# Kernel optimization log

Hardware: AMD Instinct MI355X
Metric: run time of the kernel (lower is better)

The kernel has to match this reference:

```python
import jax, jax.numpy as jnp
import numpy as np

B, T, F = 8192, 30, 16
H1, H2 = 64, 32


def _lstm(x, Wih, Whh, b):
    """PyTorch-convention LSTM (gate order i,f,g,o). x: [B,T,I] -> (ys [B,T,H], hT [B,H])."""
    H = Whh.shape[1]
    h0 = jnp.zeros((x.shape[0], H), x.dtype)

    def step(carry, xt):
        h, c = carry
        z = xt @ Wih.T + h @ Whh.T + b  # [B,4H]
        i, f, g, o = jnp.split(z, 4, axis=-1)
        c = jax.nn.sigmoid(f) * c + jax.nn.sigmoid(i) * jnp.tanh(g)
        h = jax.nn.sigmoid(o) * jnp.tanh(c)
        return (h, c), h

    (hT, _), ys = jax.lax.scan(step, (h0, h0), jnp.swapaxes(x, 0, 1))
    return jnp.swapaxes(ys, 0, 1), hT


def setup_inputs() -> dict:
    key = jax.random.key(0)
    ks = jax.random.split(key, 16)
    s = 0.1  # small init scale for numerical sanity
    return {
        "x": jax.random.normal(ks[0], (B, T, F), jnp.float32),
        "Wih1": jax.random.normal(ks[1], (4 * H1, F), jnp.float32) * s,
        "Whh1": jax.random.normal(ks[2], (4 * H1, H1), jnp.float32) * s,
        "b1": jax.random.normal(ks[3], (4 * H1,), jnp.float32) * s,
        "Wih2": jax.random.normal(ks[4], (4 * H2, H1), jnp.float32) * s,
        "Whh2": jax.random.normal(ks[5], (4 * H2, H2), jnp.float32) * s,
        "b2": jax.random.normal(ks[6], (4 * H2,), jnp.float32) * s,
        "Wih3": jax.random.normal(ks[7], (4 * H2, H2), jnp.float32) * s,
        "Whh3": jax.random.normal(ks[8], (4 * H2, H2), jnp.float32) * s,
        "b3": jax.random.normal(ks[9], (4 * H2,), jnp.float32) * s,
        "Wih4": jax.random.normal(ks[10], (4 * H1, H2), jnp.float32) * s,
        "Whh4": jax.random.normal(ks[11], (4 * H1, H1), jnp.float32) * s,
        "b4": jax.random.normal(ks[12], (4 * H1,), jnp.float32) * s,
        "Wout": jax.random.normal(ks[13], (F, H1), jnp.float32) * s,
        "bout": jax.random.normal(ks[14], (F,), jnp.float32) * s,
    }


def reference(x, Wih1, Whh1, b1, Wih2, Whh2, b2, Wih3, Whh3, b3, Wih4, Whh4, b4, Wout, bout):
    ys1, _ = _lstm(x, Wih1, Whh1, b1)          # encoder LSTM(64)
    _, latent = _lstm(ys1, Wih2, Whh2, b2)      # encoder LSTM(32) -> final hidden [B,32]
    repeated = jnp.broadcast_to(latent[:, None, :], (latent.shape[0], T, latent.shape[1]))
    ys3, _ = _lstm(repeated, Wih3, Whh3, b3)    # decoder LSTM(32)
    ys4, _ = _lstm(ys3, Wih4, Whh4, b4)         # decoder LSTM(64)
    return ys4 @ Wout.T + bout                  # [B,T,F]
```

## Files before the change

### kernel.cpp

```cpp
#include <hip/hip_runtime.h>


#define TT 30
#define FF 16
#define NT 768

typedef unsigned short u16t;
typedef __attribute__((ext_vector_type(8))) short short8;
typedef __attribute__((ext_vector_type(4))) short short4v;
typedef __attribute__((ext_vector_type(4))) float floatx4;

#define MFMA(a, b, c) __builtin_amdgcn_mfma_f32_16x16x32_bf16(a, b, c, 0, 0, 0)

#if __has_builtin(__builtin_amdgcn_exp2f)
#define EXP2(x) __builtin_amdgcn_exp2f(x)
#else
#define EXP2(x) exp2f(x)
#endif

template <int P> struct IC { static constexpr int v = P; };

__device__ __forceinline__ float rcpf(float v) { return __builtin_amdgcn_rcpf(v); }
__device__ __forceinline__ u16t f2bf(float f) {
  unsigned int u = __float_as_uint(f);
  u = (u + 0x7FFFu + ((u >> 16) & 1u)) >> 16;
  return (u16t)u;
}
__device__ __forceinline__ short8 ldFragS(const float* p, float s) {
  const float4 lo = *(const float4*)p;
  const float4 hi = *(const float4*)(p + 4);
  short8 r;
  r[0] = (short)f2bf(lo.x * s); r[1] = (short)f2bf(lo.y * s);
  r[2] = (short)f2bf(lo.z * s); r[3] = (short)f2bf(lo.w * s);
  r[4] = (short)f2bf(hi.x * s); r[5] = (short)f2bf(hi.y * s);
  r[6] = (short)f2bf(hi.z * s); r[7] = (short)f2bf(hi.w * s);
  return r;
}
__device__ __forceinline__ float cellUp(const floatx4 acc, float& c) {
  float ei = EXP2(-acc[0]);
  float ef = EXP2(-acc[1]);
  float eg = EXP2(-acc[2]);
  float eo = EXP2(-acc[3]);
  float fv = rcpf(1.f + ef);
  float P  = (1.f - eg) * rcpf((1.f + ei) * (1.f + eg));
  c = fv * c + P;
  float ec = EXP2(-2.885390082f * c);
  return (1.f - ec) * rcpf((1.f + eo) * (1.f + ec));
}

__global__ __launch_bounds__(NT, 3) void lstm_ae_mfma8(
    const float* __restrict__ x,
    const float* __restrict__ Wih1, const float* __restrict__ Whh1, const float* __restrict__ b1,
    const float* __restrict__ Wih2, const float* __restrict__ Whh2, const float* __restrict__ b2,
    const float* __restrict__ Wih3, const float* __restrict__ Whh3, const float* __restrict__ b3,
    const float* __restrict__ Wih4, const float* __restrict__ Whh4, const float* __restrict__ b4,
    const float* __restrict__ Wout, const float* __restrict__ bout,
    float* __restrict__ out)
{
  __shared__ __align__(16) u16t xAll[32 * 968];
  __shared__ __align__(16) u16t aB[32 * 264];

  const int t = threadIdx.x;
  const int w = t >> 6, lane = t & 63;
  const int q = lane >> 4, n = lane & 15;
  const int q8 = q * 8;
  const int bBase = blockIdx.x * 32;
  const int nlo = n >> 2, ngt = n & 3;
  const int r0 = n * 264, r1 = (n + 16) * 264;
  const int x0 = n * 968, x1 = (n + 16) * 968;
  const bool isZ1 = (w < 8);
  const int u = w & 3;

  const float L1 = 1.442695041f, L2 = 2.885390082f;
  const float sA = (ngt == 2) ? L2 : L1;

  for (int i = t; i < 32 * 264; i += NT) aB[i] = 0;
  {
    const float* xb = x + (size_t)bBase * (TT * FF);
    for (int i4 = t; i4 < 3840; i4 += NT) {
      int e = i4 * 4;
      int b = e / 480, r = e - b * 480;
      int stp = r >> 4, f = r & 15;
      float4 v = *(const float4*)&xb[e];
      short4v s4 = { (short)f2bf(v.x), (short)f2bf(v.y), (short)f2bf(v.z), (short)f2bf(v.w) };
      *(short4v*)&xAll[b * 968 + stp * 32 + f] = s4;
    }
    for (int i = t; i < 15360; i += NT) {
      int b = i / 480, r = i - b * 480;
      int stp = r >> 4, f = r & 15;
      xAll[b * 968 + stp * 32 + 16 + f] = 0;
    }
  }
  const short8 z8 = { 0, 0, 0, 0, 0, 0, 0, 0 };
  short8 wAf[2][3]; floatx4 biasA[2];
  if (isZ1) {
#pragma unroll
    for (int tt = 0; tt < 2; ++tt) {
      int T = w + 8 * tt;
      int row = ngt * 64 + T * 4 + nlo;
      wAf[tt][0] = z8;
      if (q < 2) wAf[tt][0] = ldFragS(&Wih1[row * 16 + q8], sA);
      wAf[tt][1] = ldFragS(&Whh1[row * 64 + q8], sA);
      wAf[tt][2] = ldFragS(&Whh1[row * 64 + 32 + q8], sA);
#pragma unroll
      for (int r = 0; r < 4; ++r) biasA[tt][r] = b1[r * 64 + T * 4 + q] * (r == 2 ? L2 : L1);
    }
  } else {
#pragma unroll
    for (int tt = 0; tt < 2; ++tt) {
      int T = 2 * u + tt;
      int row = ngt * 32 + T * 4 + nlo;
      wAf[tt][0] = ldFragS(&Wih2[row * 64 + q8], sA);
      wAf[tt][1] = ldFragS(&Wih2[row * 64 + 32 + q8], sA);
      wAf[tt][2] = ldFragS(&Whh2[row * 32 + q8], sA);
#pragma unroll
      for (int r = 0; r < 4; ++r) biasA[tt][r] = b2[r * 32 + T * 4 + q] * (r == 2 ? L2 : L1);
    }
  }
  __syncthreads();

  float cA[2][2] = {{0.f, 0.f}, {0.f, 0.f}};
  short8 bxN[2];

  if (isZ1) {
    const short8 bx0 = *(const short8*)&xAll[x0 + q8];
    const short8 bx1 = *(const short8*)&xAll[x1 + q8];
#pragma unroll
    for (int tt = 0; tt < 2; ++tt) {
      floatx4 a0 = biasA[tt], a1 = biasA[tt];
      a0 = MFMA(wAf[tt][0], bx0, a0);
      a1 = MFMA(wAf[tt][0], bx1, a1);
      aB[r0 + (w + 8 * tt) * 4 + q] = f2bf(cellUp(a0, cA[0][tt]));
      aB[r1 + (w + 8 * tt) * 4 + q] = f2bf(cellUp(a1, cA[1][tt]));
    }
    bxN[0] = *(const short8*)&xAll[x0 + 32 + q8];
    bxN[1] = *(const short8*)&xAll[x1 + 32 + q8];
  }
  __syncthreads();

  auto stepA = [&](int st, auto pc) {
    constexpr int p = decltype(pc)::v;
    const short8 h1a0 = *(const short8*)&aB[r0 + p * 64 + q8];
    const short8 h1b0 = *(const short8*)&aB[r0 + p * 64 + 32 + q8];
    const short8 h1a1 = *(const short8*)&aB[r1 + p * 64 + q8];
    const short8 h1b1 = *(const short8*)&aB[r1 + p * 64 + 32 + q8];
    if (isZ1) {
#pragma unroll
      for (int tt = 0; tt < 2; ++tt) {
        floatx4 a0 = biasA[tt], a1 = biasA[tt];
        a0 = MFMA(wAf[tt][0], bxN[0], a0);
        a1 = MFMA(wAf[tt][0], bxN[1], a1);
        a0 = MFMA(wAf[tt][1], h1a0, a0);
        a1 = MFMA(wAf[tt][1], h1a1, a1);
        a0 = MFMA(wAf[tt][2], h1b0, a0);
        a1 = MFMA(wAf[tt][2], h1b1, a1);
        aB[r0 + (1 - p) * 64 + (w + 8 * tt) * 4 + q] = f2bf(cellUp(a0, cA[0][tt]));
        aB[r1 + (1 - p) * 64 + (w + 8 * tt) * 4 + q] = f2bf(cellUp(a1, cA[1][tt]));
      }
      const int nx = (st + 2 < TT) ? st + 2 : TT - 1;
      bxN[0] = *(const short8*)&xAll[x0 + nx * 32 + q8];
      bxN[1] = *(const short8*)&xAll[x1 + nx * 32 + q8];
    } else {
      const short8 h20 = *(const short8*)&aB[r0 + 128 + (1 - p) * 32 + q8];
      const short8 h21 = *(const short8*)&aB[r1 + 128 + (1 - p) * 32 + q8];
#pragma unroll
      for (int tt = 0; tt < 2; ++tt) {
        floatx4 a0 = biasA[tt], a1 = biasA[tt];
        a0 = MFMA(wAf[tt][0], h1a0, a0);
        a1 = MFMA(wAf[tt][0], h1a1, a1);
        a0 = MFMA(wAf[tt][1], h1b0, a0);
        a1 = MFMA(wAf[tt][1], h1b1, a1);
        a0 = MFMA(wAf[tt][2], h20, a0);
        a1 = MFMA(wAf[tt][2], h21, a1);
        aB[r0 + 128 + p * 32 + (2 * u + tt) * 4 + q] = f2bf(cellUp(a0, cA[0][tt]));
        aB[r1 + 128 + p * 32 + (2 * u + tt) * 4 + q] = f2bf(cellUp(a1, cA[1][tt]));
      }
    }
    __syncthreads();
  };
  for (int st = 0; st < 28; st += 2) { stepA(st, IC<0>{}); stepA(st + 1, IC<1>{}); }
  stepA(28, IC<0>{});
  if (!isZ1) {
    const short8 h1a0 = *(const short8*)&aB[r0 + 64 + q8];
    const short8 h1b0 = *(const short8*)&aB[r0 + 96 + q8];
    const short8 h1a1 = *(const short8*)&aB[r1 + 64 + q8];
    const short8 h1b1 = *(const short8*)&aB[r1 + 96 + q8];
    const short8 h20  = *(const short8*)&aB[r0 + 128 + q8];
    const short8 h21  = *(const short8*)&aB[r1 + 128 + q8];
#pragma unroll
    for (int tt = 0; tt < 2; ++tt) {
      floatx4 a0 = biasA[tt], a1 = biasA[tt];
      a0 = MFMA(wAf[tt][0], h1a0, a0);
      a1 = MFMA(wAf[tt][0], h1a1, a1);
      a0 = MFMA(wAf[tt][1], h1b0, a0);
      a1 = MFMA(wAf[tt][1], h1b1, a1);
      a0 = MFMA(wAf[tt][2], h20, a0);
      a1 = MFMA(wAf[tt][2], h21, a1);
      aB[r0 + 160 + (2 * u + tt) * 4 + q] = f2bf(cellUp(a0, cA[0][tt]));
      aB[r1 + 160 + (2 * u + tt) * 4 + q] = f2bf(cellUp(a1, cA[1][tt]));
    }
  }
  __syncthreads();

  short8 wBf[2][3]; floatx4 biasB[2];
  short8 wof[2]; floatx4 biasO;
  short8 blat[2];
  if (isZ1) {
#pragma unroll
    for (int tt = 0; tt < 2; ++tt) {
      int T = w + 8 * tt;
      int row = ngt * 64 + T * 4 + nlo;
      wBf[tt][0] = ldFragS(&Wih4[row * 32 + q8], sA);
      wBf[tt][1] = ldFragS(&Whh4[row * 64 + q8], sA);
      wBf[tt][2] = ldFragS(&Whh4[row * 64 + 32 + q8], sA);
#pragma unroll
      for (int r = 0; r < 4; ++r) biasB[tt][r] = b4[r * 64 + T * 4 + q] * (r == 2 ? L2 : L1);
    }
    wof[0] = ldFragS(&Wout[n * 64 + q8], 1.f);
    wof[1] = ldFragS(&Wout[n * 64 + 32 + q8], 1.f);
    biasO = *(const floatx4*)&bout[q * 4];
  } else {
#pragma unroll
    for (int tt = 0; tt < 2; ++tt) {
      int T = 2 * u + tt;
      int row = ngt * 32 + T * 4 + nlo;
      wBf[tt][0] = ldFragS(&Wih3[row * 32 + q8], sA);
      wBf[tt][1] = ldFragS(&Whh3[row * 32 + q8], sA);
#pragma unroll
      for (int r = 0; r < 4; ++r) biasB[tt][r] = b3[r * 32 + T * 4 + q] * (r == 2 ? L2 : L1);
    }
    blat[0] = *(const short8*)&aB[r0 + 160 + q8];
    blat[1] = *(const short8*)&aB[r1 + 160 + q8];
  }
  for (int i = t; i < 2048; i += NT) aB[(i >> 6) * 264 + 64 + (i & 63)] = 0;
  __syncthreads();

  float cB[2][2] = {{0.f, 0.f}, {0.f, 0.f}};

  if (!isZ1) {
#pragma unroll
    for (int tt = 0; tt < 2; ++tt) {
      floatx4 a0 = biasB[tt], a1 = biasB[tt];
      a0 = MFMA(wBf[tt][0], blat[0], a0);
      a1 = MFMA(wBf[tt][0], blat[1], a1);
      aB[r0 + 192 + (2 * u + tt) * 4 + q] = f2bf(cellUp(a0, cB[0][tt]));
      aB[r1 + 192 + (2 * u + tt) * 4 + q] = f2bf(cellUp(a1, cB[1][tt]));
    }
  }
  __syncthreads();

  auto stepB = [&](int st, auto pc) {
    constexpr int p = decltype(pc)::v;
    const short8 h30 = *(const short8*)&aB[r0 + 192 + p * 32 + q8];
    const short8 h31 = *(const short8*)&aB[r1 + 192 + p * 32 + q8];
    if (isZ1) {
      const short8 h4a0 = *(const short8*)&aB[r0 + (1 - p) * 64 + q8];
      const short8 h4b0 = *(const short8*)&aB[r0 + (1 - p) * 64 + 32 + q8];
      const short8 h4a1 = *(const short8*)&aB[r1 + (1 - p) * 64 + q8];
      const short8 h4b1 = *(const short8*)&aB[r1 + (1 - p) * 64 + 32 + q8];
#pragma unroll
      for (int tt = 0; tt < 2; ++tt) {
        floatx4 a0 = biasB[tt], a1 = biasB[tt];
        a0 = MFMA(wBf[tt][0], h30, a0);
        a1 = MFMA(wBf[tt][0], h31, a1);
        a0 = MFMA(wBf[tt][1], h4a0, a0);
        a1 = MFMA(wBf[tt][1], h4a1, a1);
        a0 = MFMA(wBf[tt][2], h4b0, a0);
        a1 = MFMA(wBf[tt][2], h4b1, a1);
        aB[r0 + p * 64 + (w + 8 * tt) * 4 + q] = f2bf(cellUp(a0, cB[0][tt]));
        aB[r1 + p * 64 + (w + 8 * tt) * 4 + q] = f2bf(cellUp(a1, cB[1][tt]));
      }
      if (st > 0 && w == ((st - 1) & 7)) {
        floatx4 y0 = biasO, y1 = biasO;
        y0 = MFMA(wof[0], h4a0, y0);
        y1 = MFMA(wof[0], h4a1, y1);
        y0 = MFMA(wof[1], h4b0, y0);
        y1 = MFMA(wof[1], h4b1, y1);
        *(floatx4*)&out[((size_t)(bBase + n) * TT + (st - 1)) * FF + q * 4] = y0;
        *(floatx4*)&out[((size_t)(bBase + n + 16) * TT + (st - 1)) * FF + q * 4] = y1;
      }
    } else {
#pragma unroll
      for (int tt = 0; tt < 2; ++tt) {
        floatx4 a0 = biasB[tt], a1 = biasB[tt];
        a0 = MFMA(wBf[tt][0], blat[0], a0);
        a1 = MFMA(wBf[tt][0], blat[1], a1);
        a0 = MFMA(wBf[tt][1], h30, a0);
        a1 = MFMA(wBf[tt][1], h31, a1);
        aB[r0 + 192 + (1 - p) * 32 + (2 * u + tt) * 4 + q] = f2bf(cellUp(a0, cB[0][tt]));
        aB[r1 + 192 + (1 - p) * 32 + (2 * u + tt) * 4 + q] = f2bf(cellUp(a1, cB[1][tt]));
      }
    }
    __syncthreads();
  };
  for (int st = 0; st < 28; st += 2) { stepB(st, IC<0>{}); stepB(st + 1, IC<1>{}); }
  stepB(28, IC<0>{});
  if (isZ1) {
    const short8 h30  = *(const short8*)&aB[r0 + 224 + q8];
    const short8 h31  = *(const short8*)&aB[r1 + 224 + q8];
    const short8 h4a0 = *(const short8*)&aB[r0 + q8];
    const short8 h4b0 = *(const short8*)&aB[r0 + 32 + q8];
    const short8 h4a1 = *(const short8*)&aB[r1 + q8];
    const short8 h4b1 = *(const short8*)&aB[r1 + 32 + q8];
#pragma unroll
    for (int tt = 0; tt < 2; ++tt) {
      floatx4 a0 = biasB[tt], a1 = biasB[tt];
      a0 = MFMA(wBf[tt][0], h30, a0);
      a1 = MFMA(wBf[tt][0], h31, a1);
      a0 = MFMA(wBf[tt][1], h4a0, a0);
      a1 = MFMA(wBf[tt][1], h4a1, a1);
      a0 = MFMA(wBf[tt][2], h4b0, a0);
      a1 = MFMA(wBf[tt][2], h4b1, a1);
      aB[r0 + 64 + (w + 8 * tt) * 4 + q] = f2bf(cellUp(a0, cB[0][tt]));
      aB[r1 + 64 + (w + 8 * tt) * 4 + q] = f2bf(cellUp(a1, cB[1][tt]));
    }
    if (w == 4) {
      floatx4 y0 = biasO, y1 = biasO;
      y0 = MFMA(wof[0], h4a0, y0);
      y1 = MFMA(wof[0], h4a1, y1);
      y0 = MFMA(wof[1], h4b0, y0);
      y1 = MFMA(wof[1], h4b1, y1);
      *(floatx4*)&out[((size_t)(bBase + n) * TT + 28) * FF + q * 4] = y0;
      *(floatx4*)&out[((size_t)(bBase + n + 16) * TT + 28) * FF + q * 4] = y1;
    }
  }
  __syncthreads();
  if (w == 5) {
    const short8 ba0 = *(const short8*)&aB[r0 + 64 + q8];
    const short8 bb0 = *(const short8*)&aB[r0 + 96 + q8];
    const short8 ba1 = *(const short8*)&aB[r1 + 64 + q8];
    const short8 bb1 = *(const short8*)&aB[r1 + 96 + q8];
    floatx4 y0 = biasO, y1 = biasO;
    y0 = MFMA(wof[0], ba0, y0);
    y1 = MFMA(wof[0], ba1, y1);
    y0 = MFMA(wof[1], bb0, y0);
    y1 = MFMA(wof[1], bb1, y1);
    *(floatx4*)&out[((size_t)(bBase + n) * TT + 29) * FF + q * 4] = y0;
    *(floatx4*)&out[((size_t)(bBase + n + 16) * TT + 29) * FF + q * 4] = y1;
  }
}

extern "C" void kernel_launch(void* const* d_in, const int* in_sizes, int n_in,
                              void* d_out, int out_size, void* d_ws, size_t ws_size,
                              hipStream_t stream) {
  const float* x    = (const float*)d_in[0];
  const float* Wih1 = (const float*)d_in[1];
  const float* Whh1 = (const float*)d_in[2];
  const float* b1   = (const float*)d_in[3];
  const float* Wih2 = (const float*)d_in[4];
  const float* Whh2 = (const float*)d_in[5];
  const float* b2   = (const float*)d_in[6];
  const float* Wih3 = (const float*)d_in[7];
  const float* Whh3 = (const float*)d_in[8];
  const float* b3   = (const float*)d_in[9];
  const float* Wih4 = (const float*)d_in[10];
  const float* Whh4 = (const float*)d_in[11];
  const float* b4   = (const float*)d_in[12];
  const float* Wout = (const float*)d_in[13];
  const float* bout = (const float*)d_in[14];
  float* out = (float*)d_out;

  const int B = in_sizes[0] / (TT * FF);
  dim3 grid(B / 32), block(NT);
  lstm_ae_mfma8<<<grid, block, 0, stream>>>(
      x, Wih1, Whh1, b1, Wih2, Whh2, b2, Wih3, Whh3, b3,
      Wih4, Whh4, b4, Wout, bout, out);
}
```

Baseline: 159.7 us.

## Hoist constant decoder input projection, pack bf16 conversions, lighten barriers

Precomputes the decoder-3 input projection (Wih3·latent + bias) once, since the repeated latent is constant across timesteps, dropping one MFMA pair per step. Replaces the per-element software bf16 rounding with the hardware packed v_cvt_pk_bf16_f32 instruction. Rewrites the cell update to use one reciprocal instead of two, and swaps __syncthreads for a waitcnt on LDS plus s_barrier only. Risks: register pressure from the hoisted accumulators, and a slightly different rounding order in the cell state.

Result: faster. 156.1 us (-2.2%).

```diff
diff --git a/kernel.cpp b/kernel.cpp
--- a/kernel.cpp
+++ b/kernel.cpp
@@ -25,6 +25,15 @@
   unsigned int u = __float_as_uint(f);
   u = (u + 0x7FFFu + ((u >> 16) & 1u)) >> 16;
   return (u16t)u;
+}
+__device__ __forceinline__ unsigned int pkbf(float a, float b) {
+  unsigned int r;
+  asm("v_cvt_pk_bf16_f32 %0, %1, %2" : "=v"(r) : "v"(a), "v"(b));
+  return r;
+}
+__device__ __forceinline__ void barLDS() {
+  asm volatile("s_waitcnt lgkmcnt(0)" ::: "memory");
+  __builtin_amdgcn_s_barrier();
 }
 __device__ __forceinline__ short8 ldFragS(const float* p, float s) {
   const float4 lo = *(const float4*)p;
@@ -41,14 +50,15 @@
   float ef = EXP2(-acc[1]);
   float eg = EXP2(-acc[2]);
   float eo = EXP2(-acc[3]);
-  float fv = rcpf(1.f + ef);
-  float P  = (1.f - eg) * rcpf((1.f + ei) * (1.f + eg));
-  c = fv * c + P;
+  float pig = (1.f + ei) * (1.f + eg);
+  float pf  = 1.f + ef;
+  float num = c * pig + (1.f - eg) * pf;
+  c = num * rcpf(pf * pig);
   float ec = EXP2(-2.885390082f * c);
   return (1.f - ec) * rcpf((1.f + eo) * (1.f + ec));
 }
 
-__global__ __launch_bounds__(NT, 3) void lstm_ae_mfma8(
+__global__ __launch_bounds__(NT, 3) void lstm_ae_mfma11(
     const float* __restrict__ x,
     const float* __restrict__ Wih1, const float* __restrict__ Whh1, const float* __restrict__ b1,
     const float* __restrict__ Wih2, const float* __restrict__ Whh2, const float* __restrict__ b2,
@@ -121,6 +131,7 @@
 
   float cA[2][2] = {{0.f, 0.f}, {0.f, 0.f}};
   short8 bxN[2];
+  float h0v[2], h1v[2];
 
   if (isZ1) {
     const short8 bx0 = *(const short8*)&xAll[x0 + q8];
@@ -130,13 +141,19 @@
       floatx4 a0 = biasA[tt], a1 = biasA[tt];
       a0 = MFMA(wAf[tt][0], bx0, a0);
       a1 = MFMA(wAf[tt][0], bx1, a1);
-      aB[r0 + (w + 8 * tt) * 4 + q] = f2bf(cellUp(a0, cA[0][tt]));
-      aB[r1 + (w + 8 * tt) * 4 + q] = f2bf(cellUp(a1, cA[1][tt]));
-    }
+      h0v[tt] = cellUp(a0, cA[0][tt]);
+      h1v[tt] = cellUp(a1, cA[1][tt]);
+    }
+    unsigned int pk0 = pkbf(h0v[0], h0v[1]);
+    unsigned int pk1 = pkbf(h1v[0], h1v[1]);
+    aB[r0 + w * 4 + q] = (u16t)pk0;
+    aB[r0 + (w + 8) * 4 + q] = (u16t)(pk0 >> 16);
+    aB[r1 + w * 4 + q] = (u16t)pk1;
+    aB[r1 + (w + 8) * 4 + q] = (u16t)(pk1 >> 16);
     bxN[0] = *(const short8*)&xAll[x0 + 32 + q8];
     bxN[1] = *(const short8*)&xAll[x1 + 32 + q8];
   }
-  __syncthreads();
+  barLDS();
 
   auto stepA = [&](int st, auto pc) {
     constexpr int p = decltype(pc)::v;
@@ -154,9 +171,15 @@
         a1 = MFMA(wAf[tt][1], h1a1, a1);
         a0 = MFMA(wAf[tt][2], h1b0, a0);
         a1 = MFMA(wAf[tt][2], h1b1, a1);
-        aB[r0 + (1 - p) * 64 + (w + 8 * tt) * 4 + q] = f2bf(cellUp(a0, cA[0][tt]));
-        aB[r1 + (1 - p) * 64 + (w + 8 * tt) * 4 + q] = f2bf(cellUp(a1, cA[1][tt]));
+        h0v[tt] = cellUp(a0, cA[0][tt]);
+        h1v[tt] = cellUp(a1, cA[1][tt]);
       }
+      unsigned int pk0 = pkbf(h0v[0], h0v[1]);
+      unsigned int pk1 = pkbf(h1v[0], h1v[1]);
+      aB[r0 + (1 - p) * 64 + w * 4 + q] = (u16t)pk0;
+      aB[r0 + (1 - p) * 64 + (w + 8) * 4 + q] = (u16t)(pk0 >> 16);
+      aB[r1 + (1 - p) * 64 + w * 4 + q] = (u16t)pk1;
+      aB[r1 + (1 - p) * 64 + (w + 8) * 4 + q] = (u16t)(pk1 >> 16);
       const int nx = (st + 2 < TT) ? st + 2 : TT - 1;
       bxN[0] = *(const short8*)&xAll[x0 + nx * 32 + q8];
       bxN[1] = *(const short8*)&xAll[x1 + nx * 32 + q8];
@@ -172,11 +195,17 @@
         a1 = MFMA(wAf[tt][1], h1b1, a1);
         a0 = MFMA(wAf[tt][2], h20, a0);
         a1 = MFMA(wAf[tt][2], h21, a1);
-        aB[r0 + 128 + p * 32 + (2 * u + tt) * 4 + q] = f2bf(cellUp(a0, cA[0][tt]));
-        aB[r1 + 128 + p * 32 + (2 * u + tt) * 4 + q] = f2bf(cellUp(a1, cA[1][tt]));
+        h0v[tt] = cellUp(a0, cA[0][tt]);
+        h1v[tt] = cellUp(a1, cA[1][tt]);
       }
-    }
-    __syncthreads();
+      unsigned int pk0 = pkbf(h0v[0], h0v[1]);
+      unsigned int pk1 = pkbf(h1v[0], h1v[1]);
+      aB[r0 + 128 + p * 32 + (2 * u) * 4 + q] = (u16t)pk0;
+      aB[r0 + 128 + p * 32 + (2 * u + 1) * 4 + q] = (u16t)(pk0 >> 16);
+      aB[r1 + 128 + p * 32 + (2 * u) * 4 + q] = (u16t)pk1;
+      aB[r1 + 128 + p * 32 + (2 * u + 1) * 4 + q] = (u16t)(pk1 >> 16);
+    }
+    barLDS();
   };
   for (int st = 0; st < 28; st += 2) { stepA(st, IC<0>{}); stepA(st + 1, IC<1>{}); }
   stepA(28, IC<0>{});
@@ -196,15 +225,21 @@
       a1 = MFMA(wAf[tt][1], h1b1, a1);
       a0 = MFMA(wAf[tt][2], h20, a0);
       a1 = MFMA(wAf[tt][2], h21, a1);
-      aB[r0 + 160 + (2 * u + tt) * 4 + q] = f2bf(cellUp(a0, cA[0][tt]));
-      aB[r1 + 160 + (2 * u + tt) * 4 + q] = f2bf(cellUp(a1, cA[1][tt]));
-    }
+      h0v[tt] = cellUp(a0, cA[0][tt]);
+      h1v[tt] = cellUp(a1, cA[1][tt]);
+    }
+    unsigned int pk0 = pkbf(h0v[0], h0v[1]);
+    unsigned int pk1 = pkbf(h1v[0], h1v[1]);
+    aB[r0 + 160 + (2 * u) * 4 + q] = (u16t)pk0;
+    aB[r0 + 160 + (2 * u + 1) * 4 + q] = (u16t)(pk0 >> 16);
+    aB[r1 + 160 + (2 * u) * 4 + q] = (u16t)pk1;
+    aB[r1 + 160 + (2 * u + 1) * 4 + q] = (u16t)(pk1 >> 16);
   }
   __syncthreads();
 
   short8 wBf[2][3]; floatx4 biasB[2];
   short8 wof[2]; floatx4 biasO;
-  short8 blat[2];
+  short8 w3h[2]; floatx4 acc3c[2][2];
   if (isZ1) {
 #pragma unroll
     for (int tt = 0; tt < 2; ++tt) {
@@ -220,17 +255,20 @@
     wof[1] = ldFragS(&Wout[n * 64 + 32 + q8], 1.f);
     biasO = *(const floatx4*)&bout[q * 4];
   } else {
+    const short8 blat0 = *(const short8*)&aB[r0 + 160 + q8];
+    const short8 blat1 = *(const short8*)&aB[r1 + 160 + q8];
 #pragma unroll
     for (int tt = 0; tt < 2; ++tt) {
       int T = 2 * u + tt;
       int row = ngt * 32 + T * 4 + nlo;
-      wBf[tt][0] = ldFragS(&Wih3[row * 32 + q8], sA);
-      wBf[tt][1] = ldFragS(&Whh3[row * 32 + q8], sA);
-#pragma unroll
-      for (int r = 0; r < 4; ++r) biasB[tt][r] = b3[r * 32 + T * 4 + q] * (r == 2 ? L2 : L1);
-    }
-    blat[0] = *(const short8*)&aB[r0 + 160 + q8];
-    blat[1] = *(const short8*)&aB[r1 + 160 + q8];
+      const short8 w3i = ldFragS(&Wih3[row * 32 + q8], sA);
+      w3h[tt] = ldFragS(&Whh3[row * 32 + q8], sA);
+      floatx4 b3v;
+#pragma unroll
+      for (int r = 0; r < 4; ++r) b3v[r] = b3[r * 32 + T * 4 + q] * (r == 2 ? L2 : L1);
+      acc3c[tt][0] = MFMA(w3i, blat0, b3v);
+      acc3c[tt][1] = MFMA(w3i, blat1, b3v);
+    }
   }
   for (int i = t; i < 2048; i += NT) aB[(i >> 6) * 264 + 64 + (i & 63)] = 0;
   __syncthreads();
@@ -240,14 +278,17 @@
   if (!isZ1) {
 #pragma unroll
     for (int tt = 0; tt < 2; ++tt) {
-      floatx4 a0 = biasB[tt], a1 = biasB[tt];
-      a0 = MFMA(wBf[tt][0], blat[0], a0);
-      a1 = MFMA(wBf[tt][0], blat[1], a1);
-      aB[r0 + 192 + (2 * u + tt) * 4 + q] = f2bf(cellUp(a0, cB[0][tt]));
-      aB[r1 + 192 + (2 * u + tt) * 4 + q] = f2bf(cellUp(a1, cB[1][tt]));
-    }
-  }
-  __syncthreads();
+      h0v[tt] = cellUp(acc3c[tt][0], cB[0][tt]);
+      h1v[tt] = cellUp(acc3c[tt][1], cB[1][tt]);
+    }
+    unsigned int pk0 = pkbf(h0v[0], h0v[1]);
+    unsigned int pk1 = pkbf(h1v[0], h1v[1]);
+    aB[r0 + 192 + (2 * u) * 4 + q] = (u16t)pk0;
+    aB[r0 + 192 + (2 * u + 1) * 4 + q] = (u16t)(pk0 >> 16);
+    aB[r1 + 192 + (2 * u) * 4 + q] = (u16t)pk1;
+    aB[r1 + 192 + (2 * u + 1) * 4 + q] = (u16t)(pk1 >> 16);
+  }
+  barLDS();
 
   auto stepB = [&](int st, auto pc) {
     constexpr int p = decltype(pc)::v;
@@ -267,9 +308,15 @@
         a1 = MFMA(wBf[tt][1], h4a1, a1);
         a0 = MFMA(wBf[tt][2], h4b0, a0);
         a1 = MFMA(wBf[tt][2], h4b1, a1);
-        aB[r0 + p * 64 + (w + 8 * tt) * 4 + q] = f2bf(cellUp(a0, cB[0][tt]));
-        aB[r1 + p * 64 + (w + 8 * tt) * 4 + q] = f2bf(cellUp(a1, cB[1][tt]));
+        h0v[tt] = cellUp(a0, cB[0][tt]);
+        h1v[tt] = cellUp(a1, cB[1][tt]);
       }
+      unsigned int pk0 = pkbf(h0v[0], h0v[1]);
+      unsigned int pk1 = pkbf(h1v[0], h1v[1]);
+      aB[r0 + p * 64 + w * 4 + q] = (u16t)pk0;
+      aB[r0 + p * 64 + (w + 8) * 4 + q] = (u16t)(pk0 >> 16);
+      aB[r1 + p * 64 + w * 4 + q] = (u16t)pk1;
+      aB[r1 + p * 64 + (w + 8) * 4 + q] = (u16t)(pk1 >> 16);
       if (st > 0 && w == ((st - 1) & 7)) {
         floatx4 y0 = biasO, y1 = biasO;
         y0 = MFMA(wof[0], h4a0, y0);
@@ -282,16 +329,19 @@
     } else {
 #pragma unroll
       for (int tt = 0; tt < 2; ++tt) {
-        floatx4 a0 = biasB[tt], a1 = biasB[tt];
-        a0 = MFMA(wBf[tt][0], blat[0], a0);
-        a1 = MFMA(wBf[tt][0], blat[1], a1);
-        a0 = MFMA(wBf[tt][1], h30, a0);
-        a1 = MFMA(wBf[tt][1], h31, a1);
-        aB[r0 + 192 + (1 - p) * 32 + (2 * u + tt) * 4 + q] = f2bf(cellUp(a0, cB[0][tt]));
-        aB[r1 + 192 + (1 - p) * 32 + (2 * u + tt) * 4 + q] = f2bf(cellUp(a1, cB[1][tt]));
+        floatx4 a0 = MFMA(w3h[tt], h30, acc3c[tt][0]);
+        floatx4 a1 = MFMA(w3h[tt], h31, acc3c[tt][1]);
+        h0v[tt] = cellUp(a0, cB[0][tt]);
+        h1v[tt] = cellUp(a1, cB[1][tt]);
       }
-    }
-    __syncthreads();
+      unsigned int pk0 = pkbf(h0v[0], h0v[1]);
+      unsigned int pk1 = pkbf(h1v[0], h1v[1]);
+      aB[r0 + 192 + (1 - p) * 32 + (2 * u) * 4 + q] = (u16t)pk0;
+      aB[r0 + 192 + (1 - p) * 32 + (2 * u + 1) * 4 + q] = (u16t)(pk0 >> 16);
+      aB[r1 + 192 + (1 - p) * 32 + (2 * u) * 4 + q] = (u16t)pk1;
+      aB[r1 + 192 + (1 - p) * 32 + (2 * u + 1) * 4 + q] = (u16t)(pk1 >> 16);
+    }
+    barLDS();
   };
   for (int st = 0; st < 28; st += 2) { stepB(st, IC<0>{}); stepB(st + 1, IC<1>{}); }
   stepB(28, IC<0>{});
@@ -311,9 +361,15 @@
       a1 = MFMA(wBf[tt][1], h4a1, a1);
       a0 = MFMA(wBf[tt][2], h4b0, a0);
       a1 = MFMA(wBf[tt][2], h4b1, a1);
-      aB[r0 + 64 + (w + 8 * tt) * 4 + q] = f2bf(cellUp(a0, cB[0][tt]));
-      aB[r1 + 64 + (w + 8 * tt) * 4 + q] = f2bf(cellUp(a1, cB[1][tt]));
-    }
+      h0v[tt] = cellUp(a0, cB[0][tt]);
+      h1v[tt] = cellUp(a1, cB[1][tt]);
+    }
+    unsigned int pk0 = pkbf(h0v[0], h0v[1]);
+    unsigned int pk1 = pkbf(h1v[0], h1v[1]);
+    aB[r0 + 64 + w * 4 + q] = (u16t)pk0;
+    aB[r0 + 64 + (w + 8) * 4 + q] = (u16t)(pk0 >> 16);
+    aB[r1 + 64 + w * 4 + q] = (u16t)pk1;
+    aB[r1 + 64 + (w + 8) * 4 + q] = (u16t)(pk1 >> 16);
     if (w == 4) {
       floatx4 y0 = biasO, y1 = biasO;
       y0 = MFMA(wof[0], h4a0, y0);
@@ -324,7 +380,7 @@
       *(floatx4*)&out[((size_t)(bBase + n + 16) * TT + 28) * FF + q * 4] = y1;
     }
   }
-  __syncthreads();
+  barLDS();
   if (w == 5) {
     const short8 ba0 = *(const short8*)&aB[r0 + 64 + q8];
     const short8 bb0 = *(const short8*)&aB[r0 + 96 + q8];
@@ -362,7 +418,7 @@
 
   const int B = in_sizes[0] / (TT * FF);
   dim3 grid(B / 32), block(NT);
-  lstm_ae_mfma8<<<grid, block, 0, stream>>>(
+  lstm_ae_mfma11<<<grid, block, 0, stream>>>(
       x, Wih1, Whh1, b1, Wih2, Whh2, b2, Wih3, Whh3, b3,
       Wih4, Whh4, b4, Wout, bout, out);
 }
```
